# Kernel optimization log

Measured on AMD Instinct MI355X. Metric: run time of the kernel, lower is better.

## Reference

```python
import jax, jax.numpy as jnp
import numpy as np

B, SQ, SK, D, H, DFF, L = 8, 1024, 1024, 512, 8, 2048, 2
HD = D // H  # head dim = 64
EPS = 1e-5


def _ln(x, g, b):
    mu = jnp.mean(x, axis=-1, keepdims=True)
    var = jnp.mean((x - mu) ** 2, axis=-1, keepdims=True)
    return (x - mu) * jax.lax.rsqrt(var + EPS) * g + b


def setup_inputs() -> dict:
    key = jax.random.key(0)
    ks = jax.random.split(key, 16)
    std = 0.02
    inp = {
        'q': jax.random.normal(ks[0], (B, SQ, D), jnp.float32),
        'k': jax.random.normal(ks[1], (B, SK, D), jnp.float32),
        'v': jax.random.normal(ks[2], (B, SK, D), jnp.float32),
        # per-layer stacked params (weights stored [in, out])
        'WQ': jax.random.normal(ks[3], (L, D, D), jnp.float32) * std,
        'bQ': jnp.zeros((L, D), jnp.float32),
        'WK': jax.random.normal(ks[4], (L, D, D), jnp.float32) * std,
        'bK': jnp.zeros((L, D), jnp.float32),
        'WV': jax.random.normal(ks[5], (L, D, D), jnp.float32) * std,
        'bV': jnp.zeros((L, D), jnp.float32),
        'WO': jax.random.normal(ks[6], (L, D, D), jnp.float32) * std,
        'bO': jnp.zeros((L, D), jnp.float32),
        'Wf1': jax.random.normal(ks[7], (L, D, DFF), jnp.float32) * std,
        'bf1': jnp.zeros((L, DFF), jnp.float32),
        'Wf2': jax.random.normal(ks[8], (L, DFF, D), jnp.float32) * std,
        'bf2': jnp.zeros((L, D), jnp.float32),
        'ln1_g': jnp.ones((L, D), jnp.float32),
        'ln1_b': jnp.zeros((L, D), jnp.float32),
        'ln2_g': jnp.ones((L, D), jnp.float32),
        'ln2_b': jnp.zeros((L, D), jnp.float32),
        'scale': jnp.full((L,), HD ** -0.5, jnp.float32),       # self.scale init
        'extra_scale': jnp.ones((L,), jnp.float32),             # self.extra_scale init
        'gate_attn': jnp.ones((L,), jnp.float32),
        'gate_ffn': jnp.ones((L,), jnp.float32),
    }
    return inp


def reference(q, k, v, WQ, bQ, WK, bK, WV, bV, WO, bO, Wf1, bf1, Wf2, bf2,
              ln1_g, ln1_b, ln2_g, ln2_b, scale, extra_scale, gate_attn, gate_ffn):
    prev = None  # Realformer residual attention scores
    for i in range(L):
        # QKV projections -> [B, H, S, HD]
        qh = (jnp.einsum('bsd,de->bse', q, WQ[i]) + bQ[i]).reshape(B, SQ, H, HD).transpose(0, 2, 1, 3)
        kh = (jnp.einsum('bsd,de->bse', k, WK[i]) + bK[i]).reshape(B, SK, H, HD).transpose(0, 2, 1, 3)
        vh = (jnp.einsum('bsd,de->bse', v, WV[i]) + bV[i]).reshape(B, SK, H, HD).transpose(0, 2, 1, 3)
        eff_scale = scale[i] * jnp.clip(extra_scale[i], 0.01, 50.0)
        scores = jnp.einsum('bhqd,bhkd->bhqk', qh, kh) * eff_scale  # [B,H,SQ,SK]
        if prev is not None:
            scores = scores + prev
        attn = jax.nn.softmax(scores, axis=-1)
        out = jnp.einsum('bhqk,bhkd->bhqd', attn, vh)
        out = out.transpose(0, 2, 1, 3).reshape(B, SQ, D)
        out = jnp.einsum('bsd,de->bse', out, WO[i]) + bO[i]
        # gated residual + post-norm
        q = q + jax.nn.softplus(gate_attn[i]) * out
        q = _ln(q, ln1_g[i], ln1_b[i])
        # FFN (exact gelu like torch default)
        ff = jax.nn.gelu(jnp.einsum('bsd,df->bsf', q, Wf1[i]) + bf1[i], approximate=False)
        ff = jnp.einsum('bsf,fd->bsd', ff, Wf2[i]) + bf2[i]
        q = q + jax.nn.softplus(gate_ffn[i]) * ff
        q = _ln(q, ln2_g[i], ln2_b[i])
        prev = scores
    return q
```

## Files before the change

kernel.cpp:

```cpp
#include <hip/hip_runtime.h>

#define B_   8
#define SQ_  1024
#define SK_  1024
#define D_   512
#define H_   8
#define DFF_ 2048
#define L_   2
#define HD_  64
#define M_   8192

typedef __bf16 bf16;
using bf16x8 = __attribute__((ext_vector_type(8))) __bf16;
using f32x4  = __attribute__((ext_vector_type(4))) float;

__device__ inline f32x4 mfma16(bf16x8 a, bf16x8 b, f32x4 c) {
  return __builtin_amdgcn_mfma_f32_16x16x32_bf16(a, b, c, 0, 0, 0);
}

__device__ __forceinline__ void gl2lds16(const bf16* g, bf16* l) {
  __builtin_amdgcn_global_load_lds(
      (const __attribute__((address_space(1))) void*)g,
      (__attribute__((address_space(3))) void*)l, 16, 0, 0);
}

__global__ __launch_bounds__(256) void transpose_k(
    const float* __restrict__ in, bf16* __restrict__ out, int R, int C) {
  __shared__ bf16 tile[32][33];
  const float* inp  = in  + (size_t)blockIdx.z * R * C;
  bf16*        outp = out + (size_t)blockIdx.z * R * C;
  int c0 = blockIdx.x * 32, r0 = blockIdx.y * 32;
  int tx = threadIdx.x & 31, ty = threadIdx.x >> 5;
#pragma unroll
  for (int i = 0; i < 32; i += 8)
    tile[ty + i][tx] = (bf16)inp[(size_t)(r0 + ty + i) * C + c0 + tx];
  __syncthreads();
#pragma unroll
  for (int i = 0; i < 32; i += 8)
    outp[(size_t)(c0 + ty + i) * R + r0 + tx] = tile[tx][ty + i];
}

__global__ __launch_bounds__(256) void f2b_k(const float* __restrict__ in,
                                             bf16* __restrict__ out, int n) {
  int i = (blockIdx.x * 256 + threadIdx.x) * 4;
  if (i < n) {
    float4 v = *(const float4*)&in[i];
    out[i] = (bf16)v.x; out[i + 1] = (bf16)v.y;
    out[i + 2] = (bf16)v.z; out[i + 3] = (bf16)v.w;
  }
}

template<int BN>
__global__ __launch_bounds__(256) void gemm_t(
    const bf16* __restrict__ A, const bf16* __restrict__ Bt,
    const float* __restrict__ bias, bf16* __restrict__ Cb,
    float* __restrict__ Cf, int Nsz, int Ksz, int gelu) {
  constexpr int NI = BN / 32;
  __shared__ bf16 As[128 * 32];
  __shared__ bf16 Bs[BN * 32];
  const int tid = threadIdx.x;
  const int m0 = blockIdx.x * 128, n0 = blockIdx.y * BN;
  const int w = tid >> 6, lane = tid & 63, quad = lane >> 4, l16 = lane & 15;
  const int wm = (w & 1) << 6, wn = (w >> 1) * (BN / 2);
  const int r4 = lane >> 2;
  const int k8 = (lane & 3) * 8;
  f32x4 acc[4][NI] = {};
  for (int k0 = 0; k0 < Ksz; k0 += 32) {
    __syncthreads();
    gl2lds16(&A[(size_t)(m0 + w * 16 + r4) * Ksz + k0 + k8],
             &As[(w * 16) * 32]);
    gl2lds16(&A[(size_t)(m0 + (w + 4) * 16 + r4) * Ksz + k0 + k8],
             &As[((w + 4) * 16) * 32]);
    gl2lds16(&Bt[(size_t)(n0 + w * 16 + r4) * Ksz + k0 + k8],
             &Bs[(w * 16) * 32]);
    if constexpr (BN == 128)
      gl2lds16(&Bt[(size_t)(n0 + (w + 4) * 16 + r4) * Ksz + k0 + k8],
               &Bs[((w + 4) * 16) * 32]);
    __syncthreads();
    bf16x8 af[4], bfr[NI];
#pragma unroll
    for (int i = 0; i < 4; i++)
      af[i] = *(const bf16x8*)&As[(wm + i * 16 + l16) * 32 + quad * 8];
#pragma unroll
    for (int i = 0; i < NI; i++)
      bfr[i] = *(const bf16x8*)&Bs[(wn + i * 16 + l16) * 32 + quad * 8];
#pragma unroll
    for (int mi = 0; mi < 4; mi++)
#pragma unroll
      for (int ni = 0; ni < NI; ni++)
        acc[mi][ni] = mfma16(af[mi], bfr[ni], acc[mi][ni]);
  }
#pragma unroll
  for (int mi = 0; mi < 4; mi++)
#pragma unroll
    for (int ni = 0; ni < NI; ni++) {
      int col = n0 + wn + ni * 16 + l16;
      float bv = bias[col];
#pragma unroll
      for (int r = 0; r < 4; r++) {
        int row = m0 + wm + mi * 16 + quad * 4 + r;
        float x = acc[mi][ni][r] + bv;
        if (gelu) x = 0.5f * x * (1.0f + erff(x * 0.70710678118f));
        size_t idx = (size_t)row * Nsz + col;
        if (Cb) Cb[idx] = (bf16)x;
        if (Cf) Cf[idx] = x;
      }
    }
}

__global__ __launch_bounds__(256) void vtrans_k(const bf16* __restrict__ vh,
                                                int vstride, int coloff,
                                                bf16* __restrict__ vt) {
  __shared__ bf16 sm[64][72];
  int kt = blockIdx.x, bh = blockIdx.y;
  int b = bh >> 3, h = bh & 7;
  int tid = threadIdx.x;
  for (int c = tid; c < 512; c += 256) {
    int key = c >> 3, off = (c & 7) * 8;
    *(uint4*)&sm[key][off] = *(const uint4*)
        &vh[(size_t)(b * SK_ + kt * 64 + key) * vstride + coloff + h * 64 + off];
  }
  __syncthreads();
  for (int c = tid; c < 512; c += 256) {
    int hd = c >> 3, koff = (c & 7) * 8;
    bf16 tmp[8];
#pragma unroll
    for (int j = 0; j < 8; j++) tmp[j] = sm[koff + j][hd];
    *(uint4*)&vt[(size_t)(bh * 64 + hd) * SK_ + kt * 64 + koff] = *(uint4*)tmp;
  }
}

__global__ __launch_bounds__(256) void attn_k(
    const bf16* __restrict__ qh, const bf16* __restrict__ qh0,
    const bf16* __restrict__ kh, const bf16* __restrict__ kh0, int kstride,
    const bf16* __restrict__ vt, const float* __restrict__ scale,
    const float* __restrict__ extra, int li, bf16* __restrict__ ctx) {
  __shared__ bf16 Ks[64 * 72];
  __shared__ bf16 K0s[64 * 72];
  __shared__ bf16 Vs[64 * 72];
  __shared__ bf16 Ps[4][16 * 72];
  int qt = blockIdx.x, bh = blockIdx.y;
  int b = bh >> 3, h = bh & 7;
  int tid = threadIdx.x, w = tid >> 6, lane = tid & 63;
  int quad = lane >> 4, l16 = lane & 15;
  float eff1 = scale[li] * fminf(fmaxf(extra[li], 0.01f), 50.0f);
  float eff0 = (li > 0) ? scale[li - 1] * fminf(fmaxf(extra[li - 1], 0.01f), 50.0f) : 0.f;
  int qrow = b * SQ_ + qt * 64 + w * 16 + l16;
  const bf16* qp = qh + (size_t)qrow * D_ + h * 64 + quad * 8;
  bf16x8 aq[2] = { *(const bf16x8*)qp, *(const bf16x8*)(qp + 32) };
#pragma unroll
  for (int k2 = 0; k2 < 2; k2++)
#pragma unroll
    for (int j = 0; j < 8; j++) aq[k2][j] = (bf16)((float)aq[k2][j] * eff1);
  bf16x8 aq0[2] = {};
  if (li > 0) {
    const bf16* qp0 = qh0 + (size_t)qrow * D_ + h * 64 + quad * 8;
    aq0[0] = *(const bf16x8*)qp0; aq0[1] = *(const bf16x8*)(qp0 + 32);
#pragma unroll
    for (int k2 = 0; k2 < 2; k2++)
#pragma unroll
      for (int j = 0; j < 8; j++) aq0[k2][j] = (bf16)((float)aq0[k2][j] * eff0);
  }
  bf16x8 ones;
#pragma unroll
  for (int j = 0; j < 8; j++) ones[j] = (bf16)1.0f;

  f32x4 o[4] = {};
  f32x4 ol = {};

  for (int kt = 0; kt < SK_ / 64; kt++) {
    __syncthreads();
    for (int c = tid; c < 512; c += 256) {
      int key = c >> 3, off = (c & 7) * 8;
      size_t gk = (size_t)(b * SK_ + kt * 64 + key) * kstride + h * 64 + off;
      *(uint4*)&Ks[key * 72 + off] = *(const uint4*)&kh[gk];
      if (li > 0) *(uint4*)&K0s[key * 72 + off] = *(const uint4*)&kh0[gk];
      *(uint4*)&Vs[key * 72 + off] =
          *(const uint4*)&vt[(size_t)(bh * 64 + key) * SK_ + kt * 64 + off];
    }
    __syncthreads();
#pragma unroll
    for (int ni = 0; ni < 4; ni++) {
      const bf16* kp = &Ks[(ni * 16 + l16) * 72 + quad * 8];
      f32x4 t = {};
      t = mfma16(aq[0], *(const bf16x8*)kp, t);
      t = mfma16(aq[1], *(const bf16x8*)(kp + 32), t);
      if (li > 0) {
        const bf16* kp0 = &K0s[(ni * 16 + l16) * 72 + quad * 8];
        t = mfma16(aq0[0], *(const bf16x8*)kp0, t);
        t = mfma16(aq0[1], *(const bf16x8*)(kp0 + 32), t);
      }
#pragma unroll
      for (int r = 0; r < 4; r++)
        Ps[w][(quad * 4 + r) * 72 + ni * 16 + l16] = (bf16)__expf(t[r]);
    }
#pragma unroll
    for (int kk = 0; kk < 2; kk++) {
      bf16x8 ap = *(const bf16x8*)&Ps[w][l16 * 72 + quad * 8 + kk * 32];
      ol = mfma16(ap, ones, ol);
#pragma unroll
      for (int ni = 0; ni < 4; ni++) {
        bf16x8 bv = *(const bf16x8*)&Vs[(ni * 16 + l16) * 72 + quad * 8 + kk * 32];
        o[ni] = mfma16(ap, bv, o[ni]);
      }
    }
  }
#pragma unroll
  for (int ni = 0; ni < 4; ni++)
#pragma unroll
    for (int r = 0; r < 4; r++) {
      int row = b * SQ_ + qt * 64 + w * 16 + quad * 4 + r;
      ctx[(size_t)row * D_ + h * 64 + ni * 16 + l16] = (bf16)(o[ni][r] / ol[r]);
    }
}

__global__ __launch_bounds__(256) void ln_k(
    const float* __restrict__ cur_in, const float* __restrict__ add,
    const float* __restrict__ gate, const float* __restrict__ g,
    const float* __restrict__ bb, float* __restrict__ outf,
    bf16* __restrict__ outb) {
  int row = blockIdx.x, tid = threadIdx.x;
  float gv = gate[0];
  float sp = gv > 20.f ? gv : log1pf(expf(gv));
  size_t base = (size_t)row * D_;
  int c0 = tid * 2;
  float2 c2 = *(const float2*)&cur_in[base + c0];
  float2 a2 = *(const float2*)&add[base + c0];
  float x0 = c2.x + sp * a2.x, x1 = c2.y + sp * a2.y;
  float s = x0 + x1, s2 = x0 * x0 + x1 * x1;
#pragma unroll
  for (int m = 1; m < 64; m <<= 1) {
    s += __shfl_xor(s, m);
    s2 += __shfl_xor(s2, m);
  }
  __shared__ float sa[4], sb[4];
  int w = tid >> 6;
  if ((tid & 63) == 0) { sa[w] = s; sb[w] = s2; }
  __syncthreads();
  s = sa[0] + sa[1] + sa[2] + sa[3];
  s2 = sb[0] + sb[1] + sb[2] + sb[3];
  float mu = s * (1.f / D_);
  float var = s2 * (1.f / D_) - mu * mu;
  float rs = rsqrtf(var + 1e-5f);
  float y0 = (x0 - mu) * rs * g[c0] + bb[c0];
  float y1 = (x1 - mu) * rs * g[c0 + 1] + bb[c0 + 1];
  if (outf) { float2 y; y.x = y0; y.y = y1; *(float2*)&outf[base + c0] = y; }
  if (outb) { outb[base + c0] = (bf16)y0; outb[base + c0 + 1] = (bf16)y1; }
}

extern "C" void kernel_launch(void* const* d_in, const int* in_sizes, int n_in,
                              void* d_out, int out_size, void* d_ws,
                              size_t ws_size, hipStream_t stream) {
  const float* qin = (const float*)d_in[0];
  const float* kin = (const float*)d_in[1];
  const float* vin = (const float*)d_in[2];
  const float* WQ  = (const float*)d_in[3];
  const float* bQ  = (const float*)d_in[4];
  const float* WK  = (const float*)d_in[5];
  const float* bK  = (const float*)d_in[6];
  const float* WV  = (const float*)d_in[7];
  const float* bV  = (const float*)d_in[8];
  const float* WO  = (const float*)d_in[9];
  const float* bO  = (const float*)d_in[10];
  const float* Wf1 = (const float*)d_in[11];
  const float* bf1 = (const float*)d_in[12];
  const float* Wf2 = (const float*)d_in[13];
  const float* bf2 = (const float*)d_in[14];
  const float* l1g = (const float*)d_in[15];
  const float* l1b = (const float*)d_in[16];
  const float* l2g = (const float*)d_in[17];
  const float* l2b = (const float*)d_in[18];
  const float* sc  = (const float*)d_in[19];
  const float* ex  = (const float*)d_in[20];
  const float* ga  = (const float*)d_in[21];
  const float* gf  = (const float*)d_in[22];

  char* p = (char*)d_ws;
  auto alloc = [&](size_t bytes) {
    void* r = (void*)p;
    p += (bytes + 255) & ~(size_t)255;
    return r;
  };
  bf16* WQt  = (bf16*)alloc((size_t)L_ * D_ * D_ * 2);
  bf16* WKt  = (bf16*)alloc((size_t)L_ * D_ * D_ * 2);
  bf16* WVt  = (bf16*)alloc((size_t)L_ * D_ * D_ * 2);
  bf16* WOt  = (bf16*)alloc((size_t)L_ * D_ * D_ * 2);
  bf16* Wf1t = (bf16*)alloc((size_t)L_ * D_ * DFF_ * 2);
  bf16* Wf2t = (bf16*)alloc((size_t)L_ * D_ * DFF_ * 2);
  float* cur  = (float*)alloc((size_t)M_ * D_ * 4);
  bf16* curb  = (bf16*)alloc((size_t)M_ * D_ * 2);
  bf16* qb    = (bf16*)alloc((size_t)M_ * D_ * 2);
  bf16* kb    = (bf16*)alloc((size_t)M_ * D_ * 2);
  bf16* vb    = (bf16*)alloc((size_t)M_ * D_ * 2);
  bf16* khh   = (bf16*)alloc((size_t)M_ * 2 * D_ * 2);
  bf16* vhh   = (bf16*)alloc((size_t)M_ * 2 * D_ * 2);
  bf16* qh0b  = (bf16*)alloc((size_t)M_ * D_ * 2);
  bf16* qh1b  = (bf16*)alloc((size_t)M_ * D_ * 2);
  bf16* vt0   = (bf16*)alloc((size_t)M_ * D_ * 2);
  bf16* vt1   = (bf16*)alloc((size_t)M_ * D_ * 2);
  bf16* ctx   = (bf16*)alloc((size_t)M_ * D_ * 2);
  float* proj = (float*)alloc((size_t)M_ * D_ * 4);
  bf16* ffmid = (bf16*)alloc((size_t)M_ * DFF_ * 2);
  float* ffout = (float*)alloc((size_t)M_ * D_ * 4);

  transpose_k<<<dim3(D_ / 32, D_ / 32, L_), 256, 0, stream>>>(WQ, WQt, D_, D_);
  transpose_k<<<dim3(D_ / 32, D_ / 32, L_), 256, 0, stream>>>(WK, WKt, D_, D_);
  transpose_k<<<dim3(D_ / 32, D_ / 32, L_), 256, 0, stream>>>(WV, WVt, D_, D_);
  transpose_k<<<dim3(D_ / 32, D_ / 32, L_), 256, 0, stream>>>(WO, WOt, D_, D_);
  transpose_k<<<dim3(DFF_ / 32, D_ / 32, L_), 256, 0, stream>>>(Wf1, Wf1t, D_, DFF_);
  transpose_k<<<dim3(D_ / 32, DFF_ / 32, L_), 256, 0, stream>>>(Wf2, Wf2t, DFF_, D_);
  f2b_k<<<(M_ * D_) / 1024, 256, 0, stream>>>(qin, qb, M_ * D_);
  f2b_k<<<(M_ * D_) / 1024, 256, 0, stream>>>(kin, kb, M_ * D_);
  f2b_k<<<(M_ * D_) / 1024, 256, 0, stream>>>(vin, vb, M_ * D_);

  gemm_t<64><<<dim3(M_ / 128, 16), 256, 0, stream>>>(
      kb, WKt, bK, khh, nullptr, 2 * D_, D_, 0);
  gemm_t<64><<<dim3(M_ / 128, 16), 256, 0, stream>>>(
      vb, WVt, bV, vhh, nullptr, 2 * D_, D_, 0);
  vtrans_k<<<dim3(SK_ / 64, B_ * H_), 256, 0, stream>>>(vhh, 2 * D_, 0, vt0);
  vtrans_k<<<dim3(SK_ / 64, B_ * H_), 256, 0, stream>>>(vhh, 2 * D_, D_, vt1);
  gemm_t<64><<<dim3(M_ / 128, 8), 256, 0, stream>>>(
      qb, WQt, bQ, qh0b, nullptr, D_, D_, 0);

  for (int li = 0; li < L_; li++) {
    if (li > 0)
      gemm_t<64><<<dim3(M_ / 128, 8), 256, 0, stream>>>(
          curb, WQt + (size_t)li * D_ * D_, bQ + li * D_, qh1b, nullptr, D_, D_, 0);
    attn_k<<<dim3(SQ_ / 64, B_ * H_), 256, 0, stream>>>(
        (li == 0) ? qh0b : qh1b, qh0b, khh + (size_t)li * D_, khh, 2 * D_,
        (li == 0) ? vt0 : vt1, sc, ex, li, ctx);
    gemm_t<64><<<dim3(M_ / 128, 8), 256, 0, stream>>>(
        ctx, WOt + (size_t)li * D_ * D_, bO + li * D_, nullptr, proj, D_, D_, 0);
    ln_k<<<M_, 256, 0, stream>>>((li == 0) ? qin : cur, proj, ga + li,
                                 l1g + li * D_, l1b + li * D_, cur, curb);
    gemm_t<128><<<dim3(M_ / 128, DFF_ / 128), 256, 0, stream>>>(
        curb, Wf1t + (size_t)li * D_ * DFF_, bf1 + li * DFF_, ffmid, nullptr,
        DFF_, D_, 1);
    gemm_t<64><<<dim3(M_ / 128, 8), 256, 0, stream>>>(
        ffmid, Wf2t + (size_t)li * DFF_ * D_, bf2 + li * D_, nullptr, ffout,
        D_, DFF_, 0);
    ln_k<<<M_, 256, 0, stream>>>(cur, ffout, gf + li, l2g + li * D_,
                                 l2b + li * D_,
                                 (li == L_ - 1) ? (float*)d_out : cur,
                                 (li == L_ - 1) ? nullptr : curb);
  }
}
```

Before: 596.6 us.

## Double-buffer LDS staging in GEMM and attention with async global-to-LDS loads

The GEMM and attention kernels now use two LDS buffers. The next K tile is issued before computing on the current one, and one barrier per iteration replaces two. Attention now loads K/V with direct global-to-LDS loads into a split 32-column layout, and is templated on whether the previous-layer score term exists, so the branch is resolved at compile time. The K/V projection GEMMs switch to 128-wide N tiles. The extra buffers double LDS use, and the unpadded 32-wide layout may bring back bank conflicts.

```diff
diff --git a/kernel.cpp b/kernel.cpp
--- a/kernel.cpp
+++ b/kernel.cpp
@@ -56,8 +56,8 @@
     const float* __restrict__ bias, bf16* __restrict__ Cb,
     float* __restrict__ Cf, int Nsz, int Ksz, int gelu) {
   constexpr int NI = BN / 32;
-  __shared__ bf16 As[128 * 32];
-  __shared__ bf16 Bs[BN * 32];
+  __shared__ bf16 As[2][128 * 32];
+  __shared__ bf16 Bs[2][BN * 32];
   const int tid = threadIdx.x;
   const int m0 = blockIdx.x * 128, n0 = blockIdx.y * BN;
   const int w = tid >> 6, lane = tid & 63, quad = lane >> 4, l16 = lane & 15;
@@ -65,30 +65,37 @@
   const int r4 = lane >> 2;
   const int k8 = (lane & 3) * 8;
   f32x4 acc[4][NI] = {};
-  for (int k0 = 0; k0 < Ksz; k0 += 32) {
-    __syncthreads();
+
+  auto stage = [&](int k0, int buf) {
     gl2lds16(&A[(size_t)(m0 + w * 16 + r4) * Ksz + k0 + k8],
-             &As[(w * 16) * 32]);
+             &As[buf][(w * 16) * 32]);
     gl2lds16(&A[(size_t)(m0 + (w + 4) * 16 + r4) * Ksz + k0 + k8],
-             &As[((w + 4) * 16) * 32]);
+             &As[buf][((w + 4) * 16) * 32]);
     gl2lds16(&Bt[(size_t)(n0 + w * 16 + r4) * Ksz + k0 + k8],
-             &Bs[(w * 16) * 32]);
+             &Bs[buf][(w * 16) * 32]);
     if constexpr (BN == 128)
       gl2lds16(&Bt[(size_t)(n0 + (w + 4) * 16 + r4) * Ksz + k0 + k8],
-               &Bs[((w + 4) * 16) * 32]);
-    __syncthreads();
+               &Bs[buf][((w + 4) * 16) * 32]);
+  };
+
+  stage(0, 0);
+  __syncthreads();
+  int buf = 0;
+  for (int k0 = 0; k0 < Ksz; k0 += 32, buf ^= 1) {
+    if (k0 + 32 < Ksz) stage(k0 + 32, buf ^ 1);
     bf16x8 af[4], bfr[NI];
 #pragma unroll
     for (int i = 0; i < 4; i++)
-      af[i] = *(const bf16x8*)&As[(wm + i * 16 + l16) * 32 + quad * 8];
+      af[i] = *(const bf16x8*)&As[buf][(wm + i * 16 + l16) * 32 + quad * 8];
 #pragma unroll
     for (int i = 0; i < NI; i++)
-      bfr[i] = *(const bf16x8*)&Bs[(wn + i * 16 + l16) * 32 + quad * 8];
+      bfr[i] = *(const bf16x8*)&Bs[buf][(wn + i * 16 + l16) * 32 + quad * 8];
 #pragma unroll
     for (int mi = 0; mi < 4; mi++)
 #pragma unroll
       for (int ni = 0; ni < NI; ni++)
         acc[mi][ni] = mfma16(af[mi], bfr[ni], acc[mi][ni]);
+    __syncthreads();
   }
 #pragma unroll
   for (int mi = 0; mi < 4; mi++)
@@ -130,21 +137,23 @@
   }
 }
 
-__global__ __launch_bounds__(256) void attn_k(
+template<bool HAS0>
+__global__ __launch_bounds__(256) void attn_t(
     const bf16* __restrict__ qh, const bf16* __restrict__ qh0,
     const bf16* __restrict__ kh, const bf16* __restrict__ kh0, int kstride,
     const bf16* __restrict__ vt, const float* __restrict__ scale,
     const float* __restrict__ extra, int li, bf16* __restrict__ ctx) {
-  __shared__ bf16 Ks[64 * 72];
-  __shared__ bf16 K0s[64 * 72];
-  __shared__ bf16 Vs[64 * 72];
+  __shared__ bf16 Ks[2][2][64 * 32];
+  __shared__ bf16 K0s[HAS0 ? 2 : 1][2][64 * 32];
+  __shared__ bf16 Vs[2][2][64 * 32];
   __shared__ bf16 Ps[4][16 * 72];
   int qt = blockIdx.x, bh = blockIdx.y;
   int b = bh >> 3, h = bh & 7;
   int tid = threadIdx.x, w = tid >> 6, lane = tid & 63;
   int quad = lane >> 4, l16 = lane & 15;
+  const int r4 = lane >> 2, c4 = (lane & 3) * 8;
   float eff1 = scale[li] * fminf(fmaxf(extra[li], 0.01f), 50.0f);
-  float eff0 = (li > 0) ? scale[li - 1] * fminf(fmaxf(extra[li - 1], 0.01f), 50.0f) : 0.f;
+  float eff0 = HAS0 ? scale[li - 1] * fminf(fmaxf(extra[li - 1], 0.01f), 50.0f) : 0.f;
   int qrow = b * SQ_ + qt * 64 + w * 16 + l16;
   const bf16* qp = qh + (size_t)qrow * D_ + h * 64 + quad * 8;
   bf16x8 aq[2] = { *(const bf16x8*)qp, *(const bf16x8*)(qp + 32) };
@@ -153,7 +162,7 @@
 #pragma unroll
     for (int j = 0; j < 8; j++) aq[k2][j] = (bf16)((float)aq[k2][j] * eff1);
   bf16x8 aq0[2] = {};
-  if (li > 0) {
+  if constexpr (HAS0) {
     const bf16* qp0 = qh0 + (size_t)qrow * D_ + h * 64 + quad * 8;
     aq0[0] = *(const bf16x8*)qp0; aq0[1] = *(const bf16x8*)(qp0 + 32);
 #pragma unroll
@@ -168,27 +177,33 @@
   f32x4 o[4] = {};
   f32x4 ol = {};
 
-  for (int kt = 0; kt < SK_ / 64; kt++) {
-    __syncthreads();
-    for (int c = tid; c < 512; c += 256) {
-      int key = c >> 3, off = (c & 7) * 8;
-      size_t gk = (size_t)(b * SK_ + kt * 64 + key) * kstride + h * 64 + off;
-      *(uint4*)&Ks[key * 72 + off] = *(const uint4*)&kh[gk];
-      if (li > 0) *(uint4*)&K0s[key * 72 + off] = *(const uint4*)&kh0[gk];
-      *(uint4*)&Vs[key * 72 + off] =
-          *(const uint4*)&vt[(size_t)(bh * 64 + key) * SK_ + kt * 64 + off];
-    }
-    __syncthreads();
+  auto stage = [&](int kt, int bufi) {
+    size_t kg = (size_t)(b * SK_ + kt * 64 + w * 16 + r4) * kstride + h * 64 + c4;
+    gl2lds16(&kh[kg],      &Ks[bufi][0][(w * 16) * 32]);
+    gl2lds16(&kh[kg + 32], &Ks[bufi][1][(w * 16) * 32]);
+    if constexpr (HAS0) {
+      gl2lds16(&kh0[kg],      &K0s[bufi][0][(w * 16) * 32]);
+      gl2lds16(&kh0[kg + 32], &K0s[bufi][1][(w * 16) * 32]);
+    }
+    size_t vg = (size_t)(bh * 64 + w * 16 + r4) * SK_ + kt * 64 + c4;
+    gl2lds16(&vt[vg],      &Vs[bufi][0][(w * 16) * 32]);
+    gl2lds16(&vt[vg + 32], &Vs[bufi][1][(w * 16) * 32]);
+  };
+
+  stage(0, 0);
+  __syncthreads();
+  int buf = 0;
+  for (int kt = 0; kt < SK_ / 64; kt++, buf ^= 1) {
+    if (kt + 1 < SK_ / 64) stage(kt + 1, buf ^ 1);
 #pragma unroll
     for (int ni = 0; ni < 4; ni++) {
-      const bf16* kp = &Ks[(ni * 16 + l16) * 72 + quad * 8];
+      int ro = (ni * 16 + l16) * 32 + quad * 8;
       f32x4 t = {};
-      t = mfma16(aq[0], *(const bf16x8*)kp, t);
-      t = mfma16(aq[1], *(const bf16x8*)(kp + 32), t);
-      if (li > 0) {
-        const bf16* kp0 = &K0s[(ni * 16 + l16) * 72 + quad * 8];
-        t = mfma16(aq0[0], *(const bf16x8*)kp0, t);
-        t = mfma16(aq0[1], *(const bf16x8*)(kp0 + 32), t);
+      t = mfma16(aq[0], *(const bf16x8*)&Ks[buf][0][ro], t);
+      t = mfma16(aq[1], *(const bf16x8*)&Ks[buf][1][ro], t);
+      if constexpr (HAS0) {
+        t = mfma16(aq0[0], *(const bf16x8*)&K0s[buf][0][ro], t);
+        t = mfma16(aq0[1], *(const bf16x8*)&K0s[buf][1][ro], t);
       }
 #pragma unroll
       for (int r = 0; r < 4; r++)
@@ -200,10 +215,11 @@
       ol = mfma16(ap, ones, ol);
 #pragma unroll
       for (int ni = 0; ni < 4; ni++) {
-        bf16x8 bv = *(const bf16x8*)&Vs[(ni * 16 + l16) * 72 + quad * 8 + kk * 32];
+        bf16x8 bv = *(const bf16x8*)&Vs[buf][kk][(ni * 16 + l16) * 32 + quad * 8];
         o[ni] = mfma16(ap, bv, o[ni]);
       }
     }
+    __syncthreads();
   }
 #pragma unroll
   for (int ni = 0; ni < 4; ni++)
@@ -313,9 +329,9 @@
   f2b_k<<<(M_ * D_) / 1024, 256, 0, stream>>>(kin, kb, M_ * D_);
   f2b_k<<<(M_ * D_) / 1024, 256, 0, stream>>>(vin, vb, M_ * D_);
 
-  gemm_t<64><<<dim3(M_ / 128, 16), 256, 0, stream>>>(
+  gemm_t<128><<<dim3(M_ / 128, 8), 256, 0, stream>>>(
       kb, WKt, bK, khh, nullptr, 2 * D_, D_, 0);
-  gemm_t<64><<<dim3(M_ / 128, 16), 256, 0, stream>>>(
+  gemm_t<128><<<dim3(M_ / 128, 8), 256, 0, stream>>>(
       vb, WVt, bV, vhh, nullptr, 2 * D_, D_, 0);
   vtrans_k<<<dim3(SK_ / 64, B_ * H_), 256, 0, stream>>>(vhh, 2 * D_, 0, vt0);
   vtrans_k<<<dim3(SK_ / 64, B_ * H_), 256, 0, stream>>>(vhh, 2 * D_, D_, vt1);
@@ -326,9 +342,12 @@
     if (li > 0)
       gemm_t<64><<<dim3(M_ / 128, 8), 256, 0, stream>>>(
           curb, WQt + (size_t)li * D_ * D_, bQ + li * D_, qh1b, nullptr, D_, D_, 0);
-    attn_k<<<dim3(SQ_ / 64, B_ * H_), 256, 0, stream>>>(
-        (li == 0) ? qh0b : qh1b, qh0b, khh + (size_t)li * D_, khh, 2 * D_,
-        (li == 0) ? vt0 : vt1, sc, ex, li, ctx);
+    if (li == 0)
+      attn_t<false><<<dim3(SQ_ / 64, B_ * H_), 256, 0, stream>>>(
+          qh0b, qh0b, khh, khh, 2 * D_, vt0, sc, ex, 0, ctx);
+    else
+      attn_t<true><<<dim3(SQ_ / 64, B_ * H_), 256, 0, stream>>>(
+          qh1b, qh0b, khh + (size_t)li * D_, khh, 2 * D_, vt1, sc, ex, 1, ctx);
     gemm_t<64><<<dim3(M_ / 128, 8), 256, 0, stream>>>(
         ctx, WOt + (size_t)li * D_ * D_, bO + li * D_, nullptr, proj, D_, D_, 0);
     ln_k<<<M_, 256, 0, stream>>>((li == 0) ? qin : cur, proj, ga + li,
```

Measured after the change: 584.5 us. -2.0%, faster.
